# Kernel tuning notes

Measured on AMD Instinct MI355X. Metric: run time of the kernel, lower is better.

The kernel has to match this reference:

```python
import jax, jax.numpy as jnp
import numpy as np

B, N, C = 16, 1024, 768
D = 512
DEPTH = 4
K = 3
HP = WP = 32
A_EPS = 1e-4
POW_MIN = 1e-20
LN_EPS = 1e-5


def setup_inputs() -> dict:
    key = jax.random.key(0)
    ks = jax.random.split(key, 20)
    inp = {
        "tokens": jax.random.normal(ks[0], (B, N, C), dtype=jnp.float32),
        "in_proj_w": jax.random.normal(ks[1], (C, D), dtype=jnp.float32) * 0.02,
        "in_proj_b": jnp.zeros((D,), dtype=jnp.float32),
        "blk_norm_w": jnp.ones((DEPTH, D), dtype=jnp.float32),
        "blk_norm_b": jnp.zeros((DEPTH, D), dtype=jnp.float32),
        "blk_inp_w": jax.random.normal(ks[2], (DEPTH, D, 2 * D), dtype=jnp.float32) * 0.02,
        "blk_inp_b": jnp.zeros((DEPTH, 2 * D), dtype=jnp.float32),
        "blk_conv_w": jax.random.normal(ks[3], (DEPTH, K, K, 1, D), dtype=jnp.float32) * 0.1,
        "blk_conv_b": jnp.zeros((DEPTH, D), dtype=jnp.float32),
        "blk_a_logit": jax.random.normal(ks[4], (DEPTH, D), dtype=jnp.float32) * 0.1,
        "blk_b": jnp.ones((DEPTH, D), dtype=jnp.float32) + jax.random.normal(ks[5], (DEPTH, D), dtype=jnp.float32) * 0.02,
        "blk_c": jnp.ones((DEPTH, D), dtype=jnp.float32) + jax.random.normal(ks[6], (DEPTH, D), dtype=jnp.float32) * 0.02,
        "blk_d": jnp.ones((DEPTH, D), dtype=jnp.float32) + jax.random.normal(ks[7], (DEPTH, D), dtype=jnp.float32) * 0.02,
        "blk_out_w": jax.random.normal(ks[8], (DEPTH, D, D), dtype=jnp.float32) * 0.02,
        "blk_out_b": jnp.zeros((DEPTH, D), dtype=jnp.float32),
        "out_norm_w": jnp.ones((D,), dtype=jnp.float32),
        "out_norm_b": jnp.zeros((D,), dtype=jnp.float32),
    }
    return inp


def _layernorm(x, w, b):
    mu = jnp.mean(x, axis=-1, keepdims=True)
    var = jnp.var(x, axis=-1, keepdims=True)
    return (x - mu) * jax.lax.rsqrt(var + LN_EPS) * w + b


def _ssm_scan(x, a_logit, bb, cc, dd):
    # x: (B', L, D)   s_t = a s_{t-1} + b x_t ; y_t = c s_t + d x_t  (log-domain cumsum form)
    L = x.shape[1]
    a = jnp.clip(jax.nn.sigmoid(a_logit), A_EPS, 1.0 - A_EPS)
    t = jnp.arange(L, dtype=jnp.float32)
    a_pow = jnp.maximum(jnp.exp(t[:, None] * jnp.log(a)[None, :]), POW_MIN)  # (L, D)
    u = x * bb  # (B', L, D)
    r = jnp.cumsum(u / a_pow[None], axis=1)
    s = r * a_pow[None]
    return s * cc + x * dd


def _scan2d(x, a_logit, bb, cc, dd):
    # x: (B, H, W, D); bidirectional row-major + col-major scans, averaged
    Bb, H, W, Dd = x.shape
    L = H * W
    seq_row = x.reshape(Bb, L, Dd)
    seq_col = jnp.transpose(x, (0, 2, 1, 3)).reshape(Bb, L, Dd)
    seqs = jnp.concatenate([seq_row, seq_col], axis=0)            # (2B, L, D)
    all_seqs = jnp.concatenate([seqs, seqs[:, ::-1]], axis=0)     # (4B, L, D)
    y2 = _ssm_scan(all_seqs, a_logit, bb, cc, dd)
    y_f, y_rev = jnp.split(y2, 2, axis=0)
    y = 0.5 * (y_f + y_rev[:, ::-1])
    y_row, y_col = jnp.split(y, 2, axis=0)
    y_row_map = y_row.reshape(Bb, H, W, Dd)
    y_col_map = jnp.transpose(y_col.reshape(Bb, W, H, Dd), (0, 2, 1, 3))
    return 0.5 * (y_row_map + y_col_map)


def _dwconv_silu(x, kernel, bias):
    # x: (B,H,W,D); kernel: (K,K,1,D) depthwise; SAME padding (odd k)
    y = jax.lax.conv_general_dilated(
        x, kernel, window_strides=(1, 1), padding="SAME",
        feature_group_count=x.shape[-1],
        dimension_numbers=("NHWC", "HWIO", "NHWC"))
    return jax.nn.silu(y + bias)


def _block(x, nw, nb, iw, ib, cw, cb, al, sb, sc, sd, ow, ob):
    h = _layernorm(x, nw, nb)
    xg = h @ iw + ib                      # (B,H,W,2D)
    x_in, gate = jnp.split(xg, 2, axis=-1)
    gate = jax.nn.sigmoid(gate)
    u = _dwconv_silu(x_in, cw, cb)
    y = _scan2d(u, al, sb, sc, sd)
    y = (y * gate) @ ow + ob
    return x + y


def reference(tokens, in_proj_w, in_proj_b, blk_norm_w, blk_norm_b, blk_inp_w,
              blk_inp_b, blk_conv_w, blk_conv_b, blk_a_logit, blk_b, blk_c,
              blk_d, blk_out_w, blk_out_b, out_norm_w, out_norm_b):
    x = tokens @ in_proj_w + in_proj_b          # (B, N, D)
    x = x.reshape(B, HP, WP, D)                 # token grid
    for i in range(DEPTH):
        x = _block(x, blk_norm_w[i], blk_norm_b[i], blk_inp_w[i], blk_inp_b[i],
                   blk_conv_w[i], blk_conv_b[i], blk_a_logit[i], blk_b[i],
                   blk_c[i], blk_d[i], blk_out_w[i], blk_out_b[i])
    x = _layernorm(x, out_norm_w, out_norm_b)
    return jnp.mean(x, axis=(1, 2))             # pooled global vector (B, D)
```

## Files before the change

kernel.cpp:

```cpp
#include <hip/hip_runtime.h>
#include <hip/hip_bf16.h>
#include <math.h>

#define NPOS 16384
#define DD   512
#define PP   ((size_t)NPOS * DD)

typedef __bf16 bf16x8 __attribute__((ext_vector_type(8)));
typedef __bf16 bf16x4 __attribute__((ext_vector_type(4)));
typedef float  f32x4  __attribute__((ext_vector_type(4)));

__device__ __forceinline__ void g2lds16(const void* g, void* l) {
  __builtin_amdgcn_global_load_lds(
      (__attribute__((address_space(1))) void*)g,
      (__attribute__((address_space(3))) void*)l, 16, 0, 0);
}

__global__ __launch_bounds__(256, 3) void gemm_bf_k(
    const __bf16* __restrict__ A, const __bf16* __restrict__ Bt,
    const float* __restrict__ bias, const float* __restrict__ res,
    float* __restrict__ C0, __bf16* __restrict__ C1, __bf16* __restrict__ C1b,
    int N, int K, int epi)
{
  __shared__ __bf16 Asm[2][128 * 32];
  __shared__ __bf16 Bsm[2][128 * 32];
  const int tid  = threadIdx.x;
  const int wave = tid >> 6;
  const int lane = tid & 63;
  const int quad = lane >> 4;
  const int l16  = lane & 15;
  const int bm = blockIdx.x * 128;
  const int bn = blockIdx.y * 128;
  const int wm = (wave >> 1) << 6;
  const int wn = (wave & 1) << 6;

  const int srow   = lane >> 2;
  const int schunk = (((lane & 3) ^ ((lane >> 3) & 3)) << 3);

  f32x4 acc[4][4];
  const f32x4 z4 = {0.f, 0.f, 0.f, 0.f};
  #pragma unroll
  for (int i = 0; i < 4; ++i)
    #pragma unroll
    for (int j = 0; j < 4; ++j) acc[i][j] = z4;

  const __bf16* Ab = A  + (size_t)bm * K;
  const __bf16* Bb = Bt + (size_t)bn * K;
  const int nk = K >> 5;

  #define STAGE(buf, kb)                                                              \
    {                                                                                 \
      const int k0s = (kb) << 5;                                                      \
      _Pragma("unroll")                                                               \
      for (int c = 0; c < 2; ++c) {                                                   \
        const int cc = wave * 2 + c;                                                  \
        g2lds16(Ab + (size_t)(cc * 16 + srow) * K + k0s + schunk, &Asm[buf][cc * 512]);\
        g2lds16(Bb + (size_t)(cc * 16 + srow) * K + k0s + schunk, &Bsm[buf][cc * 512]);\
      }                                                                               \
    }

  STAGE(0, 0)
  int cur = 0;
  for (int kb = 0; kb < nk; ++kb) {
    __syncthreads();
    if (kb + 1 < nk) STAGE(cur ^ 1, kb + 1)
    bf16x8 af[4], bg[4];
    #pragma unroll
    for (int i = 0; i < 4; ++i) {
      int m = wm + i * 16 + l16;
      af[i] = *(const bf16x8*)(&Asm[cur][m * 32 + ((quad ^ ((m >> 1) & 3)) << 3)]);
    }
    #pragma unroll
    for (int j = 0; j < 4; ++j) {
      int n = wn + j * 16 + l16;
      bg[j] = *(const bf16x8*)(&Bsm[cur][n * 32 + ((quad ^ ((n >> 1) & 3)) << 3)]);
    }
    #pragma unroll
    for (int i = 0; i < 4; ++i)
      #pragma unroll
      for (int j = 0; j < 4; ++j)
        acc[i][j] = __builtin_amdgcn_mfma_f32_16x16x32_bf16(af[i], bg[j], acc[i][j], 0, 0, 0);
    cur ^= 1;
  }
  #undef STAGE

  const bool dosig = (epi == 1) && (bn >= 512);
  #pragma unroll
  for (int j = 0; j < 4; ++j) {
    const int col = wn + j * 16 + l16;
    const float bv = bias[bn + col];
    #pragma unroll
    for (int i = 0; i < 4; ++i) {
      const int row0 = bm + wm + i * 16 + quad * 4;
      #pragma unroll
      for (int r = 0; r < 4; ++r) {
        float v = acc[i][j][r] + bv;
        if (epi == 1) {
          if (dosig) {
            v = 1.f / (1.f + expf(-v));
            C1[(size_t)(row0 + r) * 512 + (bn - 512) + col] = (__bf16)v;
          } else {
            C1b[(size_t)(row0 + r) * 512 + bn + col] = (__bf16)v;
          }
        } else {
          size_t off = (size_t)(row0 + r) * N + bn + col;
          if (epi == 2) v += res[off];
          C0[off] = v;
        }
      }
    }
  }
}

__global__ __launch_bounds__(256) void cvt_k(const float* __restrict__ s, __bf16* __restrict__ d)
{
  size_t i = ((size_t)blockIdx.x * 256 + threadIdx.x) * 8;
  float4 a = *(const float4*)(s + i);
  float4 b = *(const float4*)(s + i + 4);
  bf16x8 v;
  v[0] = (__bf16)a.x; v[1] = (__bf16)a.y; v[2] = (__bf16)a.z; v[3] = (__bf16)a.w;
  v[4] = (__bf16)b.x; v[5] = (__bf16)b.y; v[6] = (__bf16)b.z; v[7] = (__bf16)b.w;
  *(bf16x8*)(d + i) = v;
}

__global__ __launch_bounds__(256) void tr_k(const float* __restrict__ src, __bf16* __restrict__ dst,
                                            int K, int N, size_t sstr, size_t dstr)
{
  __shared__ float t[32][33];
  const float* s = src + blockIdx.z * sstr;
  __bf16* d = dst + blockIdx.z * dstr;
  int n0 = blockIdx.x * 32, k0 = blockIdx.y * 32;
  int tx = threadIdx.x & 31, ty = threadIdx.x >> 5;
  #pragma unroll
  for (int i = 0; i < 4; ++i)
    t[ty + i * 8][tx] = s[(size_t)(k0 + ty + i * 8) * N + n0 + tx];
  __syncthreads();
  #pragma unroll
  for (int i = 0; i < 4; ++i)
    d[(size_t)(n0 + ty + i * 8) * K + k0 + tx] = (__bf16)t[tx][ty + i * 8];
}

__global__ __launch_bounds__(256) void ln_k(const float* __restrict__ x, const float* __restrict__ w,
                                            const float* __restrict__ bv, __bf16* __restrict__ out)
{
  int gw = (blockIdx.x * 256 + threadIdx.x) >> 6;
  int lane = threadIdx.x & 63;
  const float* xp = x + ((size_t)gw << 9) + lane * 8;
  float4 u0 = *(const float4*)xp;
  float4 u1 = *(const float4*)(xp + 4);
  float v[8] = {u0.x,u0.y,u0.z,u0.w,u1.x,u1.y,u1.z,u1.w};
  float s = 0.f;
  #pragma unroll
  for (int j = 0; j < 8; ++j) s += v[j];
  #pragma unroll
  for (int off = 32; off; off >>= 1) s += __shfl_xor(s, off, 64);
  float mu = s * (1.f/512.f);
  float q = 0.f;
  #pragma unroll
  for (int j = 0; j < 8; ++j) { float d = v[j] - mu; q += d*d; }
  #pragma unroll
  for (int off = 32; off; off >>= 1) q += __shfl_xor(q, off, 64);
  float rstd = rsqrtf(q * (1.f/512.f) + 1e-5f);
  int dch = lane * 8;
  float4 w0 = *(const float4*)(w + dch),  w1 = *(const float4*)(w + dch + 4);
  float4 b0 = *(const float4*)(bv + dch), b1 = *(const float4*)(bv + dch + 4);
  float wv[8] = {w0.x,w0.y,w0.z,w0.w,w1.x,w1.y,w1.z,w1.w};
  float bb[8] = {b0.x,b0.y,b0.z,b0.w,b1.x,b1.y,b1.z,b1.w};
  bf16x8 ov;
  #pragma unroll
  for (int j = 0; j < 8; ++j) ov[j] = (__bf16)((v[j] - mu) * rstd * wv[j] + bb[j]);
  *(bf16x8*)(out + ((size_t)gw << 9) + dch) = ov;
}

__device__ __forceinline__ float sig_a(float al) {
  float a = 1.f / (1.f + expf(-al));
  return fminf(fmaxf(a, 1e-4f), 1.f - 1e-4f);
}

__global__ __launch_bounds__(512, 2) void scan2d_k(
    const __bf16* __restrict__ xin, const float* __restrict__ cw, const float* __restrict__ cb,
    const float* __restrict__ alog, const float* __restrict__ bvec, const float* __restrict__ cvec,
    const float* __restrict__ dvec, const __bf16* __restrict__ gate, __bf16* __restrict__ yo)
{
  __shared__ __bf16 T[32768];
  __shared__ __bf16 Y[32768];
  __shared__ float  S[4][32][32];
  const int tid = threadIdx.x;
  const int cg  = blockIdx.x;
  const int b   = blockIdx.y;
  const int ch  = tid & 31;
  const int c0  = tid >> 5;
  const int c1  = c0 + 16;
  const int d   = (cg << 5) + ch;

  const float a   = sig_a(alog[d]);
  const float lna = logf(a);
  const float ia  = 1.f / a;
  const float bb  = bvec[d];
  const float sc  = 0.25f * cvec[d];
  const float dd  = dvec[d];

  const __bf16* ub = xin + ((size_t)b << 19) + (cg << 5);

  #pragma unroll
  for (int i = 0; i < 8; ++i) {
    int flat = (tid + i * 512) << 3;
    int pos = flat >> 5;
    int c8  = flat & 31;
    *(bf16x8*)(T + flat) = *(const bf16x8*)(ub + (size_t)pos * 512 + c8);
  }
  float w00 = cw[(0 << 9) + d], w01 = cw[(1 << 9) + d], w02 = cw[(2 << 9) + d];
  float w10 = cw[(3 << 9) + d], w11 = cw[(4 << 9) + d], w12 = cw[(5 << 9) + d];
  float w20 = cw[(6 << 9) + d], w21 = cw[(7 << 9) + d], w22 = cw[(8 << 9) + d];
  const float cbv = cb[d];
  const float A0f = expf((float)(c0 << 5) * lna),        R0f = expf((float)(c0 << 5) * -lna);
  const float A1f = expf((float)(c1 << 5) * lna),        R1f = expf((float)(c1 << 5) * -lna);
  const float A0b = expf((float)((31 - c0) << 5) * lna), R0b = expf((float)((31 - c0) << 5) * -lna);
  const float A1b = expf((float)((31 - c1) << 5) * lna), R1b = expf((float)((31 - c1) << 5) * -lna);
  __syncthreads();

  {
    const bool up0 = (c0 > 0);
    const bool dn1 = (c0 < 15);
    float a0 = 0.f, a1 = 0.f, a2 = 0.f, f0 = 0.f, f1 = 0.f, f2 = 0.f;
    float b0 = up0 ? (float)T[(((c0 - 1) << 5)) * 32 + ch] : 0.f;
    float b1 =        (float)T[((c0 << 5)) * 32 + ch];
    float b2 =        (float)T[(((c0 + 1) << 5)) * 32 + ch];
    float g0 =        (float)T[(((c1 - 1) << 5)) * 32 + ch];
    float g1 =        (float)T[((c1 << 5)) * 32 + ch];
    float g2 = dn1 ? (float)T[(((c1 + 1) << 5)) * 32 + ch] : 0.f;
    #pragma unroll 4
    for (int ww = 0; ww < 32; ++ww) {
      float e0 = 0.f, e1 = 0.f, e2 = 0.f, i0 = 0.f, i1 = 0.f, i2 = 0.f;
      if (ww < 31) {
        e0 = up0 ? (float)T[(((c0 - 1) << 5) + ww + 1) * 32 + ch] : 0.f;
        e1 =        (float)T[((c0 << 5) + ww + 1) * 32 + ch];
        e2 =        (float)T[(((c0 + 1) << 5) + ww + 1) * 32 + ch];
        i0 =        (float)T[(((c1 - 1) << 5) + ww + 1) * 32 + ch];
        i1 =        (float)T[((c1 << 5) + ww + 1) * 32 + ch];
        i2 = dn1 ? (float)T[(((c1 + 1) << 5) + ww + 1) * 32 + ch] : 0.f;
      }
      float acc0 = cbv, acc1 = cbv;
      acc0 = fmaf(a0, w00, acc0); acc0 = fmaf(b0, w01, acc0); acc0 = fmaf(e0, w02, acc0);
      acc0 = fmaf(a1, w10, acc0); acc0 = fmaf(b1, w11, acc0); acc0 = fmaf(e1, w12, acc0);
      acc0 = fmaf(a2, w20, acc0); acc0 = fmaf(b2, w21, acc0); acc0 = fmaf(e2, w22, acc0);
      acc1 = fmaf(f0, w00, acc1); acc1 = fmaf(g0, w01, acc1); acc1 = fmaf(i0, w02, acc1);
      acc1 = fmaf(f1, w10, acc1); acc1 = fmaf(g1, w11, acc1); acc1 = fmaf(i1, w12, acc1);
      acc1 = fmaf(f2, w20, acc1); acc1 = fmaf(g2, w21, acc1); acc1 = fmaf(i2, w22, acc1);
      acc0 = acc0 / (1.f + expf(-acc0));
      acc1 = acc1 / (1.f + expf(-acc1));
      Y[((c0 << 5) + ww) * 32 + ch] = (__bf16)acc0;
      Y[((c1 << 5) + ww) * 32 + ch] = (__bf16)acc1;
      a0 = b0; a1 = b1; a2 = b2; b0 = e0; b1 = e1; b2 = e2;
      f0 = g0; f1 = g1; f2 = g2; g0 = i0; g1 = i1; g2 = i2;
    }
  }
  __syncthreads();

  #define STEP(r_, uu_, apr_, rp_)                                 \
    { float rr_ = (apr_ < 1e-20f) ? 1e20f : rp_;                   \
      r_ = fmaf((uu_) * bb, rr_, r_); }

  {
    float p0 = A0f, q0 = R0f, p0B = A0b, q0B = R0b;
    float p1 = A1f, q1 = R1f, p1B = A1b, q1B = R1b;
    float s0 = 0.f, s1 = 0.f, s2 = 0.f, s3 = 0.f;
    float s4 = 0.f, s5 = 0.f, s6 = 0.f, s7 = 0.f;
    #pragma unroll 4
    for (int j = 0; j < 32; ++j) {
      float u0rf = (float)Y[((c0 << 5) + j) * 32 + ch];
      float u0rb = (float)Y[((c0 << 5) + (31 - j)) * 32 + ch];
      float u0cf = (float)Y[((j << 5) | c0) * 32 + ch];
      float u0cb = (float)Y[(((31 - j) << 5) | c0) * 32 + ch];
      float u1rf = (float)Y[((c1 << 5) + j) * 32 + ch];
      float u1rb = (float)Y[((c1 << 5) + (31 - j)) * 32 + ch];
      float u1cf = (float)Y[((j << 5) | c1) * 32 + ch];
      float u1cb = (float)Y[(((31 - j) << 5) | c1) * 32 + ch];
      STEP(s0, u0rf, p0, q0)  STEP(s2, u0cf, p0, q0)
      STEP(s1, u0rb, p0B, q0B) STEP(s3, u0cb, p0B, q0B)
      STEP(s4, u1rf, p1, q1)  STEP(s6, u1cf, p1, q1)
      STEP(s5, u1rb, p1B, q1B) STEP(s7, u1cb, p1B, q1B)
      p0 *= a; q0 *= ia; p0B *= a; q0B *= ia;
      p1 *= a; q1 *= ia; p1B *= a; q1B *= ia;
    }
    S[0][c0][ch] = s0; S[1][c0][ch] = s1; S[2][c0][ch] = s2; S[3][c0][ch] = s3;
    S[0][c1][ch] = s4; S[1][c1][ch] = s5; S[2][c1][ch] = s6; S[3][c1][ch] = s7;
  }
  __syncthreads();

  if (tid < 128) {
    int arr = tid >> 5, ch2 = tid & 31;
    float run = 0.f;
    if ((arr & 1) == 0) {
      #pragma unroll 4
      for (int cc = 0; cc < 32; ++cc) { float v = S[arr][cc][ch2]; S[arr][cc][ch2] = run; run += v; }
    } else {
      #pragma unroll 4
      for (int cc = 31; cc >= 0; --cc) { float v = S[arr][cc][ch2]; S[arr][cc][ch2] = run; run += v; }
    }
  }
  __syncthreads();

  {
    float r0 = S[2][c0][ch], r1 = S[2][c1][ch];
    float p0 = A0f, q0 = R0f, p1 = A1f, q1 = R1f;
    #pragma unroll 4
    for (int j = 0; j < 32; ++j) {
      int i0 = ((j << 5) | c0) * 32 + ch, i1 = ((j << 5) | c1) * 32 + ch;
      float u0 = (float)Y[i0], u1 = (float)Y[i1];
      float ap0 = fmaxf(p0, 1e-20f), ap1 = fmaxf(p1, 1e-20f);
      STEP(r0, u0, p0, q0) STEP(r1, u1, p1, q1)
      T[i0] = (__bf16)(r0 * ap0);
      T[i1] = (__bf16)(r1 * ap1);
      p0 *= a; q0 *= ia; p1 *= a; q1 *= ia;
    }
  }
  {
    float r0 = S[3][c0][ch], r1 = S[3][c1][ch];
    float p0 = A0b, q0 = R0b, p1 = A1b, q1 = R1b;
    #pragma unroll 4
    for (int j = 31; j >= 0; --j) {
      int i0 = ((j << 5) | c0) * 32 + ch, i1 = ((j << 5) | c1) * 32 + ch;
      float u0 = (float)Y[i0], u1 = (float)Y[i1];
      float ap0 = fmaxf(p0, 1e-20f), ap1 = fmaxf(p1, 1e-20f);
      STEP(r0, u0, p0, q0) STEP(r1, u1, p1, q1)
      T[i0] = (__bf16)(sc * ((float)T[i0] + r0 * ap0));
      T[i1] = (__bf16)(sc * ((float)T[i1] + r1 * ap1));
      p0 *= a; q0 *= ia; p1 *= a; q1 *= ia;
    }
  }
  __syncthreads();

  {
    float r0 = S[0][c0][ch], r1 = S[0][c1][ch];
    float p0 = A0f, q0 = R0f, p1 = A1f, q1 = R1f;
    #pragma unroll 4
    for (int j = 0; j < 32; ++j) {
      int i0 = ((c0 << 5) + j) * 32 + ch, i1 = ((c1 << 5) + j) * 32 + ch;
      float u0 = (float)Y[i0], u1 = (float)Y[i1];
      float ap0 = fmaxf(p0, 1e-20f), ap1 = fmaxf(p1, 1e-20f);
      STEP(r0, u0, p0, q0) STEP(r1, u1, p1, q1)
      T[i0] = (__bf16)((float)T[i0] + sc * (r0 * ap0));
      T[i1] = (__bf16)((float)T[i1] + sc * (r1 * ap1));
      p0 *= a; q0 *= ia; p1 *= a; q1 *= ia;
    }
  }
  {
    const __bf16* gb = gate + ((size_t)b << 19) + (cg << 5) + ch;
    __bf16* yb = yo + ((size_t)b << 19) + (cg << 5) + ch;
    float r0 = S[1][c0][ch], r1 = S[1][c1][ch];
    float p0 = A0b, q0 = R0b, p1 = A1b, q1 = R1b;
    #pragma unroll 4
    for (int j = 31; j >= 0; --j) {
      int pp0 = (c0 << 5) + j, pp1 = (c1 << 5) + j;
      int i0 = pp0 * 32 + ch, i1 = pp1 * 32 + ch;
      float u0 = (float)Y[i0], u1 = (float)Y[i1];
      float ap0 = fmaxf(p0, 1e-20f), ap1 = fmaxf(p1, 1e-20f);
      STEP(r0, u0, p0, q0) STEP(r1, u1, p1, q1)
      float y0 = (float)T[i0] + sc * (r0 * ap0) + dd * u0;
      float y1 = (float)T[i1] + sc * (r1 * ap1) + dd * u1;
      yb[(size_t)pp0 * 512] = (__bf16)(y0 * (float)gb[(size_t)pp0 * 512]);
      yb[(size_t)pp1 * 512] = (__bf16)(y1 * (float)gb[(size_t)pp1 * 512]);
      p0 *= a; q0 *= ia; p1 *= a; q1 *= ia;
    }
  }
  #undef STEP
}

__global__ __launch_bounds__(256) void reduce_k(const __bf16* __restrict__ hn, float* __restrict__ out)
{
  __shared__ float part[4][64];
  int l = threadIdx.x & 63;
  int q = threadIdx.x >> 6;
  int d = blockIdx.y * 64 + l;
  int b = blockIdx.x;
  const __bf16* p = hn + ((size_t)b << 19) + d + ((size_t)(q * 256) << 9);
  float s0 = 0.f, s1 = 0.f, s2 = 0.f, s3 = 0.f;
  for (int t = 0; t < 256; t += 4) {
    s0 += (float)p[(size_t)(t+0) << 9];
    s1 += (float)p[(size_t)(t+1) << 9];
    s2 += (float)p[(size_t)(t+2) << 9];
    s3 += (float)p[(size_t)(t+3) << 9];
  }
  part[q][l] = (s0 + s1) + (s2 + s3);
  __syncthreads();
  if (threadIdx.x < 64)
    out[b * 512 + d] = (part[0][l] + part[1][l] + part[2][l] + part[3][l]) * (1.f / 1024.f);
}

extern "C" void kernel_launch(void* const* d_in, const int* in_sizes, int n_in,
                              void* d_out, int out_size, void* d_ws, size_t ws_size,
                              hipStream_t stream)
{
  const float* tokens = (const float*)d_in[0];
  const float* in_w   = (const float*)d_in[1];
  const float* in_b   = (const float*)d_in[2];
  const float* nw     = (const float*)d_in[3];
  const float* nb     = (const float*)d_in[4];
  const float* iw     = (const float*)d_in[5];
  const float* ib     = (const float*)d_in[6];
  const float* cw     = (const float*)d_in[7];
  const float* cb     = (const float*)d_in[8];
  const float* al     = (const float*)d_in[9];
  const float* bbv    = (const float*)d_in[10];
  const float* ccv    = (const float*)d_in[11];
  const float* ddv    = (const float*)d_in[12];
  const float* ow     = (const float*)d_in[13];
  const float* obv    = (const float*)d_in[14];
  const float* onw    = (const float*)d_in[15];
  const float* onb    = (const float*)d_in[16];

  float*  x     = (float*)d_ws;
  __bf16* hy16  = (__bf16*)(x + PP);
  __bf16* xin16 = hy16 + PP;
  __bf16* g16   = xin16 + PP;
  __bf16* iwT   = g16 + PP;
  __bf16* owT   = iwT + (size_t)4 * 1024 * 512;
  __bf16* tb16  = owT + (size_t)4 * 512 * 512;
  __bf16* inwT  = xin16;

  cvt_k<<<6144, 256, 0, stream>>>(tokens, tb16);
  tr_k<<<dim3(16, 24, 1), 256, 0, stream>>>(in_w, inwT, 768, 512, 0, 0);
  tr_k<<<dim3(32, 16, 4), 256, 0, stream>>>(iw, iwT, 512, 1024, (size_t)512*1024, (size_t)1024*512);
  tr_k<<<dim3(16, 16, 4), 256, 0, stream>>>(ow, owT, 512, 512, (size_t)512*512, (size_t)512*512);

  gemm_bf_k<<<dim3(128, 4), 256, 0, stream>>>(tb16, inwT, in_b, nullptr, x, nullptr, nullptr,
                                              512, 768, 0);

  for (int i = 0; i < 4; ++i) {
    ln_k<<<4096, 256, 0, stream>>>(x, nw + i*512, nb + i*512, hy16);
    gemm_bf_k<<<dim3(128, 8), 256, 0, stream>>>(hy16, iwT + (size_t)i*1024*512, ib + i*1024,
                                                nullptr, nullptr, g16, xin16, 1024, 512, 1);
    scan2d_k<<<dim3(16, 16), 512, 0, stream>>>(xin16, cw + i*9*512, cb + i*512,
                                               al + i*512, bbv + i*512, ccv + i*512,
                                               ddv + i*512, g16, hy16);
    gemm_bf_k<<<dim3(128, 4), 256, 0, stream>>>(hy16, owT + (size_t)i*512*512, obv + i*512,
                                                x, x, nullptr, nullptr, 512, 512, 2);
  }

  ln_k<<<4096, 256, 0, stream>>>(x, onw, onb, hy16);
  reduce_k<<<dim3(16, 8), 256, 0, stream>>>(hy16, (float*)d_out);
}
```

Before: 651.5 us.

## Replace direct global-to-LDS loads with register-staged prefetch pipeline in GEMM

Drops the global_load_lds async copies in the bf16 GEMM. Tiles are now loaded into registers two k-steps ahead and written to the alternate LDS buffer after the MFMAs, with one barrier per iteration. The aim is to hide global latency behind compute and keep the swizzled LDS layout. The cost is higher register pressure from the extra vector registers at 3 blocks/SM launch bounds, plus explicit ds_write instructions.

```diff
diff --git a/kernel.cpp b/kernel.cpp
--- a/kernel.cpp
+++ b/kernel.cpp
@@ -9,12 +9,6 @@
 typedef __bf16 bf16x8 __attribute__((ext_vector_type(8)));
 typedef __bf16 bf16x4 __attribute__((ext_vector_type(4)));
 typedef float  f32x4  __attribute__((ext_vector_type(4)));
-
-__device__ __forceinline__ void g2lds16(const void* g, void* l) {
-  __builtin_amdgcn_global_load_lds(
-      (__attribute__((address_space(1))) void*)g,
-      (__attribute__((address_space(3))) void*)l, 16, 0, 0);
-}
 
 __global__ __launch_bounds__(256, 3) void gemm_bf_k(
     const __bf16* __restrict__ A, const __bf16* __restrict__ Bt,
@@ -34,8 +28,10 @@
   const int wm = (wave >> 1) << 6;
   const int wn = (wave & 1) << 6;
 
-  const int srow   = lane >> 2;
-  const int schunk = (((lane & 3) ^ ((lane >> 3) & 3)) << 3);
+  const int r0 = tid >> 2;
+  const int r1 = r0 + 64;
+  const int sl = (tid & 3) << 3;
+  const int ca = (((tid & 3) ^ ((r0 >> 1) & 3)) << 3);
 
   f32x4 acc[4][4];
   const f32x4 z4 = {0.f, 0.f, 0.f, 0.f};
@@ -48,22 +44,31 @@
   const __bf16* Bb = Bt + (size_t)bn * K;
   const int nk = K >> 5;
 
-  #define STAGE(buf, kb)                                                              \
-    {                                                                                 \
-      const int k0s = (kb) << 5;                                                      \
-      _Pragma("unroll")                                                               \
-      for (int c = 0; c < 2; ++c) {                                                   \
-        const int cc = wave * 2 + c;                                                  \
-        g2lds16(Ab + (size_t)(cc * 16 + srow) * K + k0s + schunk, &Asm[buf][cc * 512]);\
-        g2lds16(Bb + (size_t)(cc * 16 + srow) * K + k0s + schunk, &Bsm[buf][cc * 512]);\
-      }                                                                               \
-    }
-
-  STAGE(0, 0)
+  bf16x8 ar0, ar1, br0, br1;
+
+  #define GLOAD(kb)                                                      \
+    {                                                                    \
+      const int k0s = (kb) << 5;                                         \
+      ar0 = *(const bf16x8*)(Ab + (size_t)r0 * K + k0s + ca);            \
+      ar1 = *(const bf16x8*)(Ab + (size_t)r1 * K + k0s + ca);            \
+      br0 = *(const bf16x8*)(Bb + (size_t)r0 * K + k0s + ca);            \
+      br1 = *(const bf16x8*)(Bb + (size_t)r1 * K + k0s + ca);            \
+    }
+  #define DSWRITE(buf)                                                   \
+    {                                                                    \
+      *(bf16x8*)(&Asm[buf][r0 * 32 + sl]) = ar0;                         \
+      *(bf16x8*)(&Asm[buf][r1 * 32 + sl]) = ar1;                         \
+      *(bf16x8*)(&Bsm[buf][r0 * 32 + sl]) = br0;                         \
+      *(bf16x8*)(&Bsm[buf][r1 * 32 + sl]) = br1;                         \
+    }
+
+  GLOAD(0)
+  DSWRITE(0)
+  if (nk > 1) GLOAD(1)
+  __syncthreads();
+
   int cur = 0;
   for (int kb = 0; kb < nk; ++kb) {
-    __syncthreads();
-    if (kb + 1 < nk) STAGE(cur ^ 1, kb + 1)
     bf16x8 af[4], bg[4];
     #pragma unroll
     for (int i = 0; i < 4; ++i) {
@@ -80,9 +85,15 @@
       #pragma unroll
       for (int j = 0; j < 4; ++j)
         acc[i][j] = __builtin_amdgcn_mfma_f32_16x16x32_bf16(af[i], bg[j], acc[i][j], 0, 0, 0);
+    if (kb + 1 < nk) {
+      DSWRITE(cur ^ 1)
+      if (kb + 2 < nk) GLOAD(kb + 2)
+    }
+    __syncthreads();
     cur ^= 1;
   }
-  #undef STAGE
+  #undef GLOAD
+  #undef DSWRITE
 
   const bool dosig = (epi == 1) && (bn >= 512);
   #pragma unroll
```

After: 640.1 us (median of 2 runs). Within noise of the previous version (-1.8%).

## Stage GEMM tiles through registers with two-deep prefetch instead of direct LDS loads

Applied to the files above, without the earlier changes.

Replaces the global_load_lds direct-to-LDS staging in the bf16 GEMM with ordinary vector global loads into registers, which are then written to LDS. The main loop is unrolled by two, with two register sets alternating, so global loads are issued two k-tiles ahead of their MFMA use. The goal is to hide global memory latency behind MFMA work more deeply. The cost is more VGPRs under the 256x3 launch bound and extra LDS write instructions, and the unrolled loop assumes an even number of k-tiles.

```diff
diff --git a/kernel.cpp b/kernel.cpp
--- a/kernel.cpp
+++ b/kernel.cpp
@@ -9,12 +9,6 @@
 typedef __bf16 bf16x8 __attribute__((ext_vector_type(8)));
 typedef __bf16 bf16x4 __attribute__((ext_vector_type(4)));
 typedef float  f32x4  __attribute__((ext_vector_type(4)));
-
-__device__ __forceinline__ void g2lds16(const void* g, void* l) {
-  __builtin_amdgcn_global_load_lds(
-      (__attribute__((address_space(1))) void*)g,
-      (__attribute__((address_space(3))) void*)l, 16, 0, 0);
-}
 
 __global__ __launch_bounds__(256, 3) void gemm_bf_k(
     const __bf16* __restrict__ A, const __bf16* __restrict__ Bt,
@@ -34,8 +28,10 @@
   const int wm = (wave >> 1) << 6;
   const int wn = (wave & 1) << 6;
 
-  const int srow   = lane >> 2;
-  const int schunk = (((lane & 3) ^ ((lane >> 3) & 3)) << 3);
+  const int r0 = tid >> 2;
+  const int r1 = r0 + 64;
+  const int sl = (tid & 3) << 3;
+  const int ca = (((tid & 3) ^ ((r0 >> 1) & 3)) << 3);
 
   f32x4 acc[4][4];
   const f32x4 z4 = {0.f, 0.f, 0.f, 0.f};
@@ -48,41 +44,73 @@
   const __bf16* Bb = Bt + (size_t)bn * K;
   const int nk = K >> 5;
 
-  #define STAGE(buf, kb)                                                              \
-    {                                                                                 \
-      const int k0s = (kb) << 5;                                                      \
+  bf16x8 Aa0, Aa1, Ab0, Ab1;
+  bf16x8 Ba0, Ba1, Bb0, Bb1;
+
+  #define GLOADA(kb)                                                     \
+    { const int k0s = (kb) << 5;                                         \
+      Aa0 = *(const bf16x8*)(Ab + (size_t)r0 * K + k0s + ca);            \
+      Aa1 = *(const bf16x8*)(Ab + (size_t)r1 * K + k0s + ca);            \
+      Ab0 = *(const bf16x8*)(Bb + (size_t)r0 * K + k0s + ca);            \
+      Ab1 = *(const bf16x8*)(Bb + (size_t)r1 * K + k0s + ca); }
+  #define GLOADB(kb)                                                     \
+    { const int k0s = (kb) << 5;                                         \
+      Ba0 = *(const bf16x8*)(Ab + (size_t)r0 * K + k0s + ca);            \
+      Ba1 = *(const bf16x8*)(Ab + (size_t)r1 * K + k0s + ca);            \
+      Bb0 = *(const bf16x8*)(Bb + (size_t)r0 * K + k0s + ca);            \
+      Bb1 = *(const bf16x8*)(Bb + (size_t)r1 * K + k0s + ca); }
+  #define DSWRITEA(buf)                                                  \
+    { *(bf16x8*)(&Asm[buf][r0 * 32 + sl]) = Aa0;                         \
+      *(bf16x8*)(&Asm[buf][r1 * 32 + sl]) = Aa1;                         \
+      *(bf16x8*)(&Bsm[buf][r0 * 32 + sl]) = Ab0;                         \
+      *(bf16x8*)(&Bsm[buf][r1 * 32 + sl]) = Ab1; }
+  #define DSWRITEB(buf)                                                  \
+    { *(bf16x8*)(&Asm[buf][r0 * 32 + sl]) = Ba0;                         \
+      *(bf16x8*)(&Asm[buf][r1 * 32 + sl]) = Ba1;                         \
+      *(bf16x8*)(&Bsm[buf][r0 * 32 + sl]) = Bb0;                         \
+      *(bf16x8*)(&Bsm[buf][r1 * 32 + sl]) = Bb1; }
+  #define MFMA(buf)                                                                   \
+    { bf16x8 af[4], bg[4];                                                            \
       _Pragma("unroll")                                                               \
-      for (int c = 0; c < 2; ++c) {                                                   \
-        const int cc = wave * 2 + c;                                                  \
-        g2lds16(Ab + (size_t)(cc * 16 + srow) * K + k0s + schunk, &Asm[buf][cc * 512]);\
-        g2lds16(Bb + (size_t)(cc * 16 + srow) * K + k0s + schunk, &Bsm[buf][cc * 512]);\
+      for (int i = 0; i < 4; ++i) {                                                   \
+        int m = wm + i * 16 + l16;                                                    \
+        af[i] = *(const bf16x8*)(&Asm[buf][m * 32 + ((quad ^ ((m >> 1) & 3)) << 3)]); \
       }                                                                               \
-    }
-
-  STAGE(0, 0)
+      _Pragma("unroll")                                                               \
+      for (int j = 0; j < 4; ++j) {                                                   \
+        int n = wn + j * 16 + l16;                                                    \
+        bg[j] = *(const bf16x8*)(&Bsm[buf][n * 32 + ((quad ^ ((n >> 1) & 3)) << 3)]); \
+      }                                                                               \
+      _Pragma("unroll")                                                               \
+      for (int i = 0; i < 4; ++i)                                                     \
+        _Pragma("unroll")                                                             \
+        for (int j = 0; j < 4; ++j)                                                   \
+          acc[i][j] = __builtin_amdgcn_mfma_f32_16x16x32_bf16(af[i], bg[j], acc[i][j], 0, 0, 0); }
+
+  GLOADA(0)
+  DSWRITEA(0)
+  GLOADA(1)
+  GLOADB(2)
+  __syncthreads();
+
   int cur = 0;
-  for (int kb = 0; kb < nk; ++kb) {
+  for (int kb = 0; kb < nk; kb += 2) {
+    if (kb + 1 < nk) DSWRITEA(cur ^ 1)
+    if (kb + 3 < nk) GLOADA(kb + 3)
+    MFMA(cur)
     __syncthreads();
-    if (kb + 1 < nk) STAGE(cur ^ 1, kb + 1)
-    bf16x8 af[4], bg[4];
-    #pragma unroll
-    for (int i = 0; i < 4; ++i) {
-      int m = wm + i * 16 + l16;
-      af[i] = *(const bf16x8*)(&Asm[cur][m * 32 + ((quad ^ ((m >> 1) & 3)) << 3)]);
-    }
-    #pragma unroll
-    for (int j = 0; j < 4; ++j) {
-      int n = wn + j * 16 + l16;
-      bg[j] = *(const bf16x8*)(&Bsm[cur][n * 32 + ((quad ^ ((n >> 1) & 3)) << 3)]);
-    }
-    #pragma unroll
-    for (int i = 0; i < 4; ++i)
-      #pragma unroll
-      for (int j = 0; j < 4; ++j)
-        acc[i][j] = __builtin_amdgcn_mfma_f32_16x16x32_bf16(af[i], bg[j], acc[i][j], 0, 0, 0);
     cur ^= 1;
-  }
-  #undef STAGE
+    if (kb + 2 < nk) DSWRITEB(cur ^ 1)
+    if (kb + 4 < nk) GLOADB(kb + 4)
+    MFMA(cur)
+    __syncthreads();
+    cur ^= 1;
+  }
+  #undef GLOADA
+  #undef GLOADB
+  #undef DSWRITEA
+  #undef DSWRITEB
+  #undef MFMA
 
   const bool dosig = (epi == 1) && (bn >= 512);
   #pragma unroll
```

Measured after the change: 670.0 us. +2.8%, slower.
